# Kernel tuning notes

Measured on AMD Instinct MI355X. Metric: run time of the kernel, lower is better.

## Reference

```python
import jax, jax.numpy as jnp
import numpy as np

N_NODES = 50000
N_EDGES = 500000
IN_CH = 128
OUT_CH = 256


def setup_inputs() -> dict:
    key = jax.random.key(0)
    k1, k2, k3, k4, k5 = jax.random.split(key, 5)
    x = jax.random.normal(k1, (N_NODES, IN_CH), dtype=jnp.float32)
    edge_index = jax.random.randint(k2, (2, N_EDGES), 0, N_NODES, dtype=jnp.int64)
    edge_weight = jax.random.normal(k3, (N_EDGES,), dtype=jnp.float32)
    # GCNConv linear weight (xavier-uniform) and bias (zeros in torch init; use randn for generality)
    limit = float(np.sqrt(6.0 / (IN_CH + OUT_CH)))
    W = jax.random.uniform(k4, (IN_CH, OUT_CH), minval=-limit, maxval=limit, dtype=jnp.float32)
    b = jnp.zeros((OUT_CH,), dtype=jnp.float32)
    return {"x": x, "W": W, "b": b, "edge_index": edge_index, "edge_weight": edge_weight}


def reference(x, W, b, edge_index, edge_weight):
    N = x.shape[0]
    # GCN wrapper applies sigmoid to edge weights before GCNConv
    ew = jax.nn.sigmoid(edge_weight)
    # gcn_norm: add self-loops with weight 1
    loop = jnp.arange(N, dtype=edge_index.dtype)
    row = jnp.concatenate([edge_index[0], loop])  # source nodes
    col = jnp.concatenate([edge_index[1], loop])  # target nodes
    w = jnp.concatenate([ew, jnp.ones((N,), dtype=x.dtype)])
    # degree on target index, symmetric normalization
    deg = jax.ops.segment_sum(w, col, num_segments=N)
    dinv = jnp.where(deg > 0, jax.lax.rsqrt(deg), jnp.zeros_like(deg))
    norm = dinv[row] * w * dinv[col]  # [E+N]
    # linear transform first (GCNConv: lin has no bias; bias added after aggregation)
    h = x @ W  # [N, OUT_CH]
    msg = h[row] * norm[:, None]  # gather + scale  [E+N, OUT_CH]
    out = jax.ops.segment_sum(msg, col, num_segments=N) + b
    return out
```

## Files before the change

### kernel.cpp

```cpp
#include <hip/hip_runtime.h>
#include <hip/hip_bf16.h>
#include <hip/hip_fp16.h>
#include <math.h>

#define NN 50000
#define NE 500000
#define IC 128
#define OC 256
#define NPAD 50176
#define NEB 1954
#define CAP 64

typedef short bf16x8 __attribute__((ext_vector_type(8)));
typedef float f32x4 __attribute__((ext_vector_type(4)));

static __device__ inline unsigned short f2b(float f) {
    __hip_bfloat16 h = __float2bfloat16(f);
    return *reinterpret_cast<unsigned short*>(&h);
}
static __device__ inline float b2f(short u) {
    unsigned v = ((unsigned)(unsigned short)u) << 16;
    return __int_as_float(v);
}
static __device__ inline float h2f(unsigned short h) {
    __half v = __ushort_as_half(h);
    return __half2float(v);
}
static __device__ inline float deg_to_di(unsigned long long dv) {
    return rsqrtf((float)(unsigned)dv * (1.0f / 16777216.0f) + 1.0f);
}

__global__ void k_pass1(const int* __restrict__ row,
                        const int* __restrict__ col,
                        const float* __restrict__ ew,
                        unsigned long long* __restrict__ deg64,
                        unsigned* __restrict__ epack,
                        const float* __restrict__ W,
                        unsigned short* __restrict__ WT) {
    int g = blockIdx.x * 256 + threadIdx.x;
    if (g < NE) {
        int c = col[g];
        float w = 1.0f / (1.0f + expf(-ew[g]));
        unsigned long long pack = (1ull << 32) | (unsigned long long)(unsigned)(w * 16777216.0f);
        unsigned long long old = atomicAdd(&deg64[c], pack);
        int ord = (int)(old >> 32);
        if (ord < CAP) {
            unsigned short wh = __half_as_ushort(__float2half_rn(w));
            unsigned p = ((unsigned)wh << 16) | (unsigned)row[g];
            epack[(size_t)c * CAP + ord] = p;
        }
    }
    if (g < IC * OC) {
        int k = g >> 8;
        int n = g & 255;
        WT[n * IC + k] = f2b(W[g]);
    }
}

__global__ __launch_bounds__(256) void k_scale(
        const unsigned long long* __restrict__ deg64,
        const float* __restrict__ x,
        unsigned short* __restrict__ xb) {
    int t = threadIdx.x;
    int n = blockIdx.x * 16 + (t >> 4);
    int l = t & 15;
    float di = deg_to_di(deg64[n]);
    const float4* xr = (const float4*)(x + (size_t)n * IC + l * 8);
    float4 a0 = xr[0], a1 = xr[1];
    bf16x8 o;
    o[0] = (short)f2b(a0.x * di); o[1] = (short)f2b(a0.y * di);
    o[2] = (short)f2b(a0.z * di); o[3] = (short)f2b(a0.w * di);
    o[4] = (short)f2b(a1.x * di); o[5] = (short)f2b(a1.y * di);
    o[6] = (short)f2b(a1.z * di); o[7] = (short)f2b(a1.w * di);
    ((bf16x8*)xb)[(size_t)n * 16 + l] = o;
}

__global__ __launch_bounds__(256) void k_gather_gemm(
        const unsigned short* __restrict__ xb,
        const unsigned long long* __restrict__ deg64,
        const unsigned* __restrict__ epack,
        const unsigned short* __restrict__ WT,
        const float* __restrict__ bias,
        float* __restrict__ out) {
    __shared__ __align__(16) unsigned short a[32][136];

    const int base = blockIdx.x * 32;
    const int g = threadIdx.x >> 3;
    const int l8 = threadIdx.x & 7;
    const int n = base + g;
    const bf16x8* xv = (const bf16x8*)xb;

    float acc[16];
    if (n < NN) {
        unsigned long long dv = deg64[n];
        float di = deg_to_di(dv);
        int cnt = (int)(dv >> 32);
        if (cnt > CAP) cnt = CAP;

        bf16x8 xs0 = xv[(size_t)n * 16 + l8];
        bf16x8 xs1 = xv[(size_t)n * 16 + 8 + l8];
        #pragma unroll
        for (int c = 0; c < 8; ++c) { acc[c] = b2f(xs0[c]) * di; acc[8 + c] = b2f(xs1[c]) * di; }

        const unsigned* ep = epack + (size_t)n * CAP;
        uint4 q = *(const uint4*)ep;
        int e = 0;
        for (; e + 4 <= cnt; e += 4) {
            uint4 cur = q;
            q = *(const uint4*)(ep + e + 4);
            int r0 = (int)(cur.x & 0xFFFFu);
            int r1 = (int)(cur.y & 0xFFFFu);
            int r2 = (int)(cur.z & 0xFFFFu);
            int r3 = (int)(cur.w & 0xFFFFu);
            float w0 = h2f((unsigned short)(cur.x >> 16)) * di;
            float w1 = h2f((unsigned short)(cur.y >> 16)) * di;
            float w2 = h2f((unsigned short)(cur.z >> 16)) * di;
            float w3 = h2f((unsigned short)(cur.w >> 16)) * di;
            bf16x8 v00 = xv[(size_t)r0 * 16 + l8];
            bf16x8 v01 = xv[(size_t)r0 * 16 + 8 + l8];
            bf16x8 v10 = xv[(size_t)r1 * 16 + l8];
            bf16x8 v11 = xv[(size_t)r1 * 16 + 8 + l8];
            bf16x8 v20 = xv[(size_t)r2 * 16 + l8];
            bf16x8 v21 = xv[(size_t)r2 * 16 + 8 + l8];
            bf16x8 v30 = xv[(size_t)r3 * 16 + l8];
            bf16x8 v31 = xv[(size_t)r3 * 16 + 8 + l8];
            #pragma unroll
            for (int c = 0; c < 8; ++c) { acc[c] += b2f(v00[c]) * w0; acc[8 + c] += b2f(v01[c]) * w0; }
            #pragma unroll
            for (int c = 0; c < 8; ++c) { acc[c] += b2f(v10[c]) * w1; acc[8 + c] += b2f(v11[c]) * w1; }
            #pragma unroll
            for (int c = 0; c < 8; ++c) { acc[c] += b2f(v20[c]) * w2; acc[8 + c] += b2f(v21[c]) * w2; }
            #pragma unroll
            for (int c = 0; c < 8; ++c) { acc[c] += b2f(v30[c]) * w3; acc[8 + c] += b2f(v31[c]) * w3; }
        }
        for (; e < cnt; ++e) {
            unsigned p = ep[e];
            int r = (int)(p & 0xFFFFu);
            float w = h2f((unsigned short)(p >> 16)) * di;
            bf16x8 v0 = xv[(size_t)r * 16 + l8];
            bf16x8 v1 = xv[(size_t)r * 16 + 8 + l8];
            #pragma unroll
            for (int c = 0; c < 8; ++c) { acc[c] += b2f(v0[c]) * w; acc[8 + c] += b2f(v1[c]) * w; }
        }
    } else {
        #pragma unroll
        for (int c = 0; c < 16; ++c) acc[c] = 0.0f;
    }

    bf16x8 o0, o1;
    #pragma unroll
    for (int c = 0; c < 8; ++c) { o0[c] = (short)f2b(acc[c]); o1[c] = (short)f2b(acc[8 + c]); }
    *(bf16x8*)(&a[g][l8 * 8]) = o0;
    *(bf16x8*)(&a[g][64 + l8 * 8]) = o1;

    __syncthreads();

    const int w = threadIdx.x >> 6;
    const int lane = threadIdx.x & 63;
    const int n0 = w * 64;
    const int lm = lane & 15;
    const int lk = (lane >> 4) * 8;

    f32x4 acc4[2][4] = {};
    #pragma unroll
    for (int ks = 0; ks < 4; ++ks) {
        const int k0 = ks * 32 + lk;
        bf16x8 wf[4], af[2];
        #pragma unroll
        for (int j = 0; j < 4; ++j)
            wf[j] = *(const bf16x8*)(WT + (size_t)(n0 + j * 16 + lm) * IC + k0);
        #pragma unroll
        for (int i = 0; i < 2; ++i)
            af[i] = *(const bf16x8*)(&a[i * 16 + lm][k0]);
        #pragma unroll
        for (int i = 0; i < 2; ++i)
            #pragma unroll
            for (int j = 0; j < 4; ++j)
                acc4[i][j] = __builtin_amdgcn_mfma_f32_16x16x32_bf16(wf[j], af[i], acc4[i][j], 0, 0, 0);
    }

    const int mcol = lane & 15;
    const int nb4 = (lane >> 4) * 4;
    #pragma unroll
    for (int i = 0; i < 2; ++i) {
        int m = base + i * 16 + mcol;
        if (m < NN) {
            #pragma unroll
            for (int j = 0; j < 4; ++j) {
                int nn = n0 + j * 16 + nb4;
                float4 bv = *(const float4*)&bias[nn];
                float4 ov;
                ov.x = acc4[i][j][0] + bv.x;
                ov.y = acc4[i][j][1] + bv.y;
                ov.z = acc4[i][j][2] + bv.z;
                ov.w = acc4[i][j][3] + bv.w;
                *(float4*)(out + (size_t)m * OC + nn) = ov;
            }
        }
    }
}

extern "C" void kernel_launch(void* const* d_in, const int* in_sizes, int n_in,
                              void* d_out, int out_size, void* d_ws, size_t ws_size,
                              hipStream_t stream) {
    const float* x  = (const float*)d_in[0];
    const float* W  = (const float*)d_in[1];
    const float* b  = (const float*)d_in[2];
    const int*   ei = (const int*)d_in[3];
    const float* ew = (const float*)d_in[4];
    const int* row = ei;
    const int* col = ei + NE;
    float* out = (float*)d_out;

    char* w0 = (char*)d_ws;
    unsigned long long* deg64 = (unsigned long long*)w0;  w0 += NPAD * 8;
    unsigned* epack = (unsigned*)w0;             w0 += ((size_t)NPAD * CAP + 128) * 4;
    unsigned short* WT   = (unsigned short*)w0;  w0 += IC * OC * 2;
    unsigned short* xb   = (unsigned short*)w0;

    hipMemsetAsync(deg64, 0, NPAD * 8, stream);
    k_pass1      <<<NEB, 256, 0, stream>>>(row, col, ew, deg64, epack, W, WT);
    k_scale      <<<NN / 16, 256, 0, stream>>>(deg64, x, xb);
    k_gather_gemm<<<(NN + 31) / 32, 256, 0, stream>>>(xb, deg64, epack, WT, b, out);
}
```

Measured before the change: 160.8 us.

## Shrink gather-GEMM blocks to 16 nodes with 128 threads and drop bounds checks

The fused gather+GEMM kernel now processes 16 nodes per block with 128 threads instead of 32 nodes with 256 threads. Each wave computes 128 output columns in two 64-column chunks for a single 16-row MFMA tile. Because 50000 is divisible by 16, the n<NN guards are removed, and launch bounds request 8 blocks per CU for more occupancy. The aim is better latency hiding in the random gather and finer load balancing. The cost is that each block reloads the WT fragments for only half as many rows.

After: 180.0 us. 11.9% more time.

```diff
diff --git a/kernel.cpp b/kernel.cpp
--- a/kernel.cpp
+++ b/kernel.cpp
@@ -75,76 +75,71 @@
     ((bf16x8*)xb)[(size_t)n * 16 + l] = o;
 }
 
-__global__ __launch_bounds__(256) void k_gather_gemm(
+__global__ __launch_bounds__(128, 8) void k_gather_gemm(
         const unsigned short* __restrict__ xb,
         const unsigned long long* __restrict__ deg64,
         const unsigned* __restrict__ epack,
         const unsigned short* __restrict__ WT,
         const float* __restrict__ bias,
         float* __restrict__ out) {
-    __shared__ __align__(16) unsigned short a[32][136];
-
-    const int base = blockIdx.x * 32;
+    __shared__ __align__(16) unsigned short a[16][136];
+
+    const int base = blockIdx.x * 16;
     const int g = threadIdx.x >> 3;
     const int l8 = threadIdx.x & 7;
     const int n = base + g;
     const bf16x8* xv = (const bf16x8*)xb;
 
+    unsigned long long dv = deg64[n];
+    float di = deg_to_di(dv);
+    int cnt = (int)(dv >> 32);
+    if (cnt > CAP) cnt = CAP;
+
+    bf16x8 xs0 = xv[(size_t)n * 16 + l8];
+    bf16x8 xs1 = xv[(size_t)n * 16 + 8 + l8];
     float acc[16];
-    if (n < NN) {
-        unsigned long long dv = deg64[n];
-        float di = deg_to_di(dv);
-        int cnt = (int)(dv >> 32);
-        if (cnt > CAP) cnt = CAP;
-
-        bf16x8 xs0 = xv[(size_t)n * 16 + l8];
-        bf16x8 xs1 = xv[(size_t)n * 16 + 8 + l8];
-        #pragma unroll
-        for (int c = 0; c < 8; ++c) { acc[c] = b2f(xs0[c]) * di; acc[8 + c] = b2f(xs1[c]) * di; }
-
-        const unsigned* ep = epack + (size_t)n * CAP;
-        uint4 q = *(const uint4*)ep;
-        int e = 0;
-        for (; e + 4 <= cnt; e += 4) {
-            uint4 cur = q;
-            q = *(const uint4*)(ep + e + 4);
-            int r0 = (int)(cur.x & 0xFFFFu);
-            int r1 = (int)(cur.y & 0xFFFFu);
-            int r2 = (int)(cur.z & 0xFFFFu);
-            int r3 = (int)(cur.w & 0xFFFFu);
-            float w0 = h2f((unsigned short)(cur.x >> 16)) * di;
-            float w1 = h2f((unsigned short)(cur.y >> 16)) * di;
-            float w2 = h2f((unsigned short)(cur.z >> 16)) * di;
-            float w3 = h2f((unsigned short)(cur.w >> 16)) * di;
-            bf16x8 v00 = xv[(size_t)r0 * 16 + l8];
-            bf16x8 v01 = xv[(size_t)r0 * 16 + 8 + l8];
-            bf16x8 v10 = xv[(size_t)r1 * 16 + l8];
-            bf16x8 v11 = xv[(size_t)r1 * 16 + 8 + l8];
-            bf16x8 v20 = xv[(size_t)r2 * 16 + l8];
-            bf16x8 v21 = xv[(size_t)r2 * 16 + 8 + l8];
-            bf16x8 v30 = xv[(size_t)r3 * 16 + l8];
-            bf16x8 v31 = xv[(size_t)r3 * 16 + 8 + l8];
-            #pragma unroll
-            for (int c = 0; c < 8; ++c) { acc[c] += b2f(v00[c]) * w0; acc[8 + c] += b2f(v01[c]) * w0; }
-            #pragma unroll
-            for (int c = 0; c < 8; ++c) { acc[c] += b2f(v10[c]) * w1; acc[8 + c] += b2f(v11[c]) * w1; }
-            #pragma unroll
-            for (int c = 0; c < 8; ++c) { acc[c] += b2f(v20[c]) * w2; acc[8 + c] += b2f(v21[c]) * w2; }
-            #pragma unroll
-            for (int c = 0; c < 8; ++c) { acc[c] += b2f(v30[c]) * w3; acc[8 + c] += b2f(v31[c]) * w3; }
-        }
-        for (; e < cnt; ++e) {
-            unsigned p = ep[e];
-            int r = (int)(p & 0xFFFFu);
-            float w = h2f((unsigned short)(p >> 16)) * di;
-            bf16x8 v0 = xv[(size_t)r * 16 + l8];
-            bf16x8 v1 = xv[(size_t)r * 16 + 8 + l8];
-            #pragma unroll
-            for (int c = 0; c < 8; ++c) { acc[c] += b2f(v0[c]) * w; acc[8 + c] += b2f(v1[c]) * w; }
-        }
-    } else {
-        #pragma unroll
-        for (int c = 0; c < 16; ++c) acc[c] = 0.0f;
+    #pragma unroll
+    for (int c = 0; c < 8; ++c) { acc[c] = b2f(xs0[c]) * di; acc[8 + c] = b2f(xs1[c]) * di; }
+
+    const unsigned* ep = epack + (size_t)n * CAP;
+    uint4 q = *(const uint4*)ep;
+    int e = 0;
+    for (; e + 4 <= cnt; e += 4) {
+        uint4 cur = q;
+        q = *(const uint4*)(ep + e + 4);
+        int r0 = (int)(cur.x & 0xFFFFu);
+        int r1 = (int)(cur.y & 0xFFFFu);
+        int r2 = (int)(cur.z & 0xFFFFu);
+        int r3 = (int)(cur.w & 0xFFFFu);
+        float w0 = h2f((unsigned short)(cur.x >> 16)) * di;
+        float w1 = h2f((unsigned short)(cur.y >> 16)) * di;
+        float w2 = h2f((unsigned short)(cur.z >> 16)) * di;
+        float w3 = h2f((unsigned short)(cur.w >> 16)) * di;
+        bf16x8 v00 = xv[(size_t)r0 * 16 + l8];
+        bf16x8 v01 = xv[(size_t)r0 * 16 + 8 + l8];
+        bf16x8 v10 = xv[(size_t)r1 * 16 + l8];
+        bf16x8 v11 = xv[(size_t)r1 * 16 + 8 + l8];
+        bf16x8 v20 = xv[(size_t)r2 * 16 + l8];
+        bf16x8 v21 = xv[(size_t)r2 * 16 + 8 + l8];
+        bf16x8 v30 = xv[(size_t)r3 * 16 + l8];
+        bf16x8 v31 = xv[(size_t)r3 * 16 + 8 + l8];
+        #pragma unroll
+        for (int c = 0; c < 8; ++c) { acc[c] += b2f(v00[c]) * w0; acc[8 + c] += b2f(v01[c]) * w0; }
+        #pragma unroll
+        for (int c = 0; c < 8; ++c) { acc[c] += b2f(v10[c]) * w1; acc[8 + c] += b2f(v11[c]) * w1; }
+        #pragma unroll
+        for (int c = 0; c < 8; ++c) { acc[c] += b2f(v20[c]) * w2; acc[8 + c] += b2f(v21[c]) * w2; }
+        #pragma unroll
+        for (int c = 0; c < 8; ++c) { acc[c] += b2f(v30[c]) * w3; acc[8 + c] += b2f(v31[c]) * w3; }
+    }
+    for (; e < cnt; ++e) {
+        unsigned p = ep[e];
+        int r = (int)(p & 0xFFFFu);
+        float w = h2f((unsigned short)(p >> 16)) * di;
+        bf16x8 v0 = xv[(size_t)r * 16 + l8];
+        bf16x8 v1 = xv[(size_t)r * 16 + 8 + l8];
+        #pragma unroll
+        for (int c = 0; c < 8; ++c) { acc[c] += b2f(v0[c]) * w; acc[8 + c] += b2f(v1[c]) * w; }
     }
 
     bf16x8 o0, o1;
@@ -157,45 +152,38 @@
 
     const int w = threadIdx.x >> 6;
     const int lane = threadIdx.x & 63;
-    const int n0 = w * 64;
     const int lm = lane & 15;
     const int lk = (lane >> 4) * 8;
-
-    f32x4 acc4[2][4] = {};
+    const int mcol = lane & 15;
+    const int nb4 = (lane >> 4) * 4;
+    const int m = base + mcol;
+
     #pragma unroll
-    for (int ks = 0; ks < 4; ++ks) {
-        const int k0 = ks * 32 + lk;
-        bf16x8 wf[4], af[2];
-        #pragma unroll
-        for (int j = 0; j < 4; ++j)
-            wf[j] = *(const bf16x8*)(WT + (size_t)(n0 + j * 16 + lm) * IC + k0);
-        #pragma unroll
-        for (int i = 0; i < 2; ++i)
-            af[i] = *(const bf16x8*)(&a[i * 16 + lm][k0]);
-        #pragma unroll
-        for (int i = 0; i < 2; ++i)
+    for (int ch = 0; ch < 2; ++ch) {
+        const int n0 = w * 128 + ch * 64;
+        f32x4 acc4[4] = {};
+        #pragma unroll
+        for (int ks = 0; ks < 4; ++ks) {
+            const int k0 = ks * 32 + lk;
+            bf16x8 wf[4];
             #pragma unroll
             for (int j = 0; j < 4; ++j)
-                acc4[i][j] = __builtin_amdgcn_mfma_f32_16x16x32_bf16(wf[j], af[i], acc4[i][j], 0, 0, 0);
-    }
-
-    const int mcol = lane & 15;
-    const int nb4 = (lane >> 4) * 4;
-    #pragma unroll
-    for (int i = 0; i < 2; ++i) {
-        int m = base + i * 16 + mcol;
-        if (m < NN) {
+                wf[j] = *(const bf16x8*)(WT + (size_t)(n0 + j * 16 + lm) * IC + k0);
+            bf16x8 af = *(const bf16x8*)(&a[lm][k0]);
             #pragma unroll
-            for (int j = 0; j < 4; ++j) {
-                int nn = n0 + j * 16 + nb4;
-                float4 bv = *(const float4*)&bias[nn];
-                float4 ov;
-                ov.x = acc4[i][j][0] + bv.x;
-                ov.y = acc4[i][j][1] + bv.y;
-                ov.z = acc4[i][j][2] + bv.z;
-                ov.w = acc4[i][j][3] + bv.w;
-                *(float4*)(out + (size_t)m * OC + nn) = ov;
-            }
+            for (int j = 0; j < 4; ++j)
+                acc4[j] = __builtin_amdgcn_mfma_f32_16x16x32_bf16(wf[j], af, acc4[j], 0, 0, 0);
+        }
+        #pragma unroll
+        for (int j = 0; j < 4; ++j) {
+            int nn = n0 + j * 16 + nb4;
+            float4 bv = *(const float4*)&bias[nn];
+            float4 ov;
+            ov.x = acc4[j][0] + bv.x;
+            ov.y = acc4[j][1] + bv.y;
+            ov.z = acc4[j][2] + bv.z;
+            ov.w = acc4[j][3] + bv.w;
+            *(float4*)(out + (size_t)m * OC + nn) = ov;
         }
     }
 }
@@ -221,5 +209,5 @@
     hipMemsetAsync(deg64, 0, NPAD * 8, stream);
     k_pass1      <<<NEB, 256, 0, stream>>>(row, col, ew, deg64, epack, W, WT);
     k_scale      <<<NN / 16, 256, 0, stream>>>(deg64, x, xb);
-    k_gather_gemm<<<(NN + 31) / 32, 256, 0, stream>>>(xb, deg64, epack, WT, b, out);
-}
+    k_gather_gemm<<<NN / 16, 128, 0, stream>>>(xb, deg64, epack, WT, b, out);
+}
```
